# Kernel optimization log

Hardware: AMD Instinct MI355X
Metric: run time of the kernel (lower is better)

The kernel has to match this reference:

```python
import jax, jax.numpy as jnp
import numpy as np

DIL = 2  # dilation of the 3x3 neighborhood (hardcoded in the torch module)
# 8 non-center neighbor offsets of a dilated 3x3 kernel
_OFFSETS = [(-DIL, -DIL), (-DIL, 0), (-DIL, DIL),
            (0, -DIL),              (0, DIL),
            (DIL, -DIL), (DIL, 0),  (DIL, DIL)]


def setup_inputs() -> dict:
    key = jax.random.key(0)
    k1, k2 = jax.random.split(key)
    shape = (16, 1, 1024, 1024)
    y_true = jax.random.uniform(k1, shape, dtype=jnp.float32)
    y_pred = jax.random.uniform(k2, shape, dtype=jnp.float32)
    return {"y_true": y_true, "y_pred": y_pred}


def reference(y_true, y_pred):
    # --- BCE with torch's log clamp at -100 (reduction='none') ---
    log_p  = jnp.maximum(jnp.log(y_pred),   -100.0)
    log_1p = jnp.maximum(jnp.log1p(-y_pred), -100.0)
    a = -(y_true * log_p + (1.0 - y_true) * log_1p)

    # --- detached copy (y_pred.clone().detach()) ---
    sloss = jax.lax.stop_gradient(y_pred)

    # --- max |center - neighbor| over 8 dilated neighbors, zero-padded borders ---
    H, W = sloss.shape[2], sloss.shape[3]
    padded = jnp.pad(sloss, ((0, 0), (0, 0), (DIL, DIL), (DIL, DIL)))
    unfolded_weights = jnp.zeros_like(sloss)
    for dy, dx in _OFFSETS:
        nb = padded[:, :, DIL + dy:DIL + dy + H, DIL + dx:DIL + dx + W]
        unfolded_weights = jnp.maximum(unfolded_weights, jnp.abs(sloss - nb))

    # thred[thred < 0.5] = 0; loss1 uses thred BEFORE the >=0.5 -> 1 assignment
    thred = jnp.where(sloss >= 0.5, sloss, 0.0)
    loss = unfolded_weights * thred + a
    return loss.mean()
```

## Files before the change

kernel.cpp:

```cpp
#include <hip/hip_runtime.h>

#define HH 1024
#define WW 1024
#define NB 16
#define NROWS (NB * HH)
#define NELEM ((long long)NROWS * WW)

__global__ __launch_bounds__(256) void closs_main(const float* __restrict__ yt,
                                                  const float* __restrict__ yp,
                                                  float* __restrict__ partial) {
    __shared__ float up[1032];
    __shared__ float ce[1032];
    __shared__ float dn[1032];

    const int r   = blockIdx.x;
    const int y   = r & (HH - 1);
    const int tid = threadIdx.x;
    const int x4  = tid << 2;
    const long long rowbase = (long long)r * WW;

    if (tid < 4) {
        up[tid] = 0.f; ce[tid] = 0.f; dn[tid] = 0.f;
        up[1028 + tid] = 0.f; ce[1028 + tid] = 0.f; dn[1028 + tid] = 0.f;
    }

    float4 c4 = ((const float4*)(yp + rowbase))[tid];
    float4 u4 = make_float4(0.f, 0.f, 0.f, 0.f);
    float4 d4 = make_float4(0.f, 0.f, 0.f, 0.f);
    if (y >= 2)      u4 = ((const float4*)(yp + rowbase - 2 * WW))[tid];
    if (y < HH - 2)  d4 = ((const float4*)(yp + rowbase + 2 * WW))[tid];
    *(float4*)&ce[4 + x4] = c4;
    *(float4*)&up[4 + x4] = u4;
    *(float4*)&dn[4 + x4] = d4;
    __syncthreads();

    float sum = 0.f;
#pragma unroll
    for (int j = 0; j < 4; ++j) {
        const int x   = tid + (j << 8);
        const int idx = 4 + x;
        const float c = ce[idx];
        const float t = yt[rowbase + x];

        float w = fabsf(c - up[idx - 2]);
        w = fmaxf(w, fabsf(c - up[idx]));
        w = fmaxf(w, fabsf(c - up[idx + 2]));
        w = fmaxf(w, fabsf(c - ce[idx - 2]));
        w = fmaxf(w, fabsf(c - ce[idx + 2]));
        w = fmaxf(w, fabsf(c - dn[idx - 2]));
        w = fmaxf(w, fabsf(c - dn[idx]));
        w = fmaxf(w, fabsf(c - dn[idx + 2]));

        const float lp  = fmaxf(__logf(c), -100.f);
        const float l1p = fmaxf(__logf(1.f - c), -100.f);
        const float a   = -(t * lp + (1.f - t) * l1p);
        const float th  = (c >= 0.5f) ? c : 0.f;
        sum += w * th + a;
    }

    for (int o = 32; o > 0; o >>= 1) sum += __shfl_down(sum, o);
    __shared__ float wsum[4];
    if ((tid & 63) == 0) wsum[tid >> 6] = sum;
    __syncthreads();
    if (tid == 0) partial[r] = wsum[0] + wsum[1] + wsum[2] + wsum[3];
}

__global__ __launch_bounds__(256) void closs_reduce(const float* __restrict__ partial,
                                                    float* __restrict__ out) {
    float s = 0.f;
    for (int i = threadIdx.x; i < NROWS; i += 256) s += partial[i];
    for (int o = 32; o > 0; o >>= 1) s += __shfl_down(s, o);
    __shared__ float wsum[4];
    if ((threadIdx.x & 63) == 0) wsum[threadIdx.x >> 6] = s;
    __syncthreads();
    if (threadIdx.x == 0)
        out[0] = (wsum[0] + wsum[1] + wsum[2] + wsum[3]) * (1.0f / (float)NELEM);
}

extern "C" void kernel_launch(void* const* d_in, const int* in_sizes, int n_in,
                              void* d_out, int out_size, void* d_ws, size_t ws_size,
                              hipStream_t stream) {
    const float* y_true = (const float*)d_in[0];
    const float* y_pred = (const float*)d_in[1];
    float* out = (float*)d_out;
    float* partial = (float*)d_ws;

    closs_main<<<NROWS, 256, 0, stream>>>(y_true, y_pred, partial);
    closs_reduce<<<1, 256, 0, stream>>>(partial, out);
}
```

Baseline: 162.7 us.

## Replace LDS staging with direct register loads of halo neighbors; vectorize final reduce

The main kernel drops the shared-memory row staging and __syncthreads. Each thread now loads its 4 contiguous elements plus 2-element halos from global memory (float2/float4) for the center, up and down rows, computes the dilated max-diff in registers, and reads y_true as a float4. The intent is to remove LDS traffic and the barrier, at the cost of some redundant, less aligned halo loads that the cache should absorb. The reduce kernel moves to 1024 threads with float4 loads to shorten the serial loop.

```diff
diff --git a/kernel.cpp b/kernel.cpp
--- a/kernel.cpp
+++ b/kernel.cpp
@@ -9,53 +9,89 @@
 __global__ __launch_bounds__(256) void closs_main(const float* __restrict__ yt,
                                                   const float* __restrict__ yp,
                                                   float* __restrict__ partial) {
-    __shared__ float up[1032];
-    __shared__ float ce[1032];
-    __shared__ float dn[1032];
-
     const int r   = blockIdx.x;
     const int y   = r & (HH - 1);
     const int tid = threadIdx.x;
-    const int x4  = tid << 2;
+    const int x0  = tid << 2;
     const long long rowbase = (long long)r * WW;
 
-    if (tid < 4) {
-        up[tid] = 0.f; ce[tid] = 0.f; dn[tid] = 0.f;
-        up[1028 + tid] = 0.f; ce[1028 + tid] = 0.f; dn[1028 + tid] = 0.f;
+    const bool has_up = (y >= 2);
+    const bool has_dn = (y < HH - 2);
+    const bool ledge  = (tid == 0);
+    const bool redge  = (tid == 255);
+
+    const int offL = ledge ? x0 : (x0 - 2);
+    const int offR = redge ? x0 : (x0 + 4);
+
+    const float* pce = yp + rowbase;
+    const float* pup = pce - 2 * WW;
+    const float* pdn = pce + 2 * WW;
+
+    float ce[8];
+    {
+        float2 a = *(const float2*)(pce + offL);
+        float4 b = *(const float4*)(pce + x0);
+        float2 c = *(const float2*)(pce + offR);
+        if (ledge) { a.x = 0.f; a.y = 0.f; }
+        if (redge) { c.x = 0.f; c.y = 0.f; }
+        ce[0]=a.x; ce[1]=a.y; ce[2]=b.x; ce[3]=b.y; ce[4]=b.z; ce[5]=b.w; ce[6]=c.x; ce[7]=c.y;
+    }
+    const float4 t4 = *(const float4*)(yt + rowbase + x0);
+
+    float w0, w1, w2, w3;
+    {
+        w0 = fmaxf(fabsf(ce[2] - ce[0]), fabsf(ce[2] - ce[4]));
+        w1 = fmaxf(fabsf(ce[3] - ce[1]), fabsf(ce[3] - ce[5]));
+        w2 = fmaxf(fabsf(ce[4] - ce[2]), fabsf(ce[4] - ce[6]));
+        w3 = fmaxf(fabsf(ce[5] - ce[3]), fabsf(ce[5] - ce[7]));
+    }
+    if (has_up) {
+        float2 a = *(const float2*)(pup + offL);
+        float4 b = *(const float4*)(pup + x0);
+        float2 c = *(const float2*)(pup + offR);
+        if (ledge) { a.x = 0.f; a.y = 0.f; }
+        if (redge) { c.x = 0.f; c.y = 0.f; }
+        float u[8] = {a.x, a.y, b.x, b.y, b.z, b.w, c.x, c.y};
+        w0 = fmaxf(w0, fmaxf(fabsf(ce[2]-u[0]), fmaxf(fabsf(ce[2]-u[2]), fabsf(ce[2]-u[4]))));
+        w1 = fmaxf(w1, fmaxf(fabsf(ce[3]-u[1]), fmaxf(fabsf(ce[3]-u[3]), fabsf(ce[3]-u[5]))));
+        w2 = fmaxf(w2, fmaxf(fabsf(ce[4]-u[2]), fmaxf(fabsf(ce[4]-u[4]), fabsf(ce[4]-u[6]))));
+        w3 = fmaxf(w3, fmaxf(fabsf(ce[5]-u[3]), fmaxf(fabsf(ce[5]-u[5]), fabsf(ce[5]-u[7]))));
+    } else {
+        w0 = fmaxf(w0, fabsf(ce[2]));
+        w1 = fmaxf(w1, fabsf(ce[3]));
+        w2 = fmaxf(w2, fabsf(ce[4]));
+        w3 = fmaxf(w3, fabsf(ce[5]));
+    }
+    if (has_dn) {
+        float2 a = *(const float2*)(pdn + offL);
+        float4 b = *(const float4*)(pdn + x0);
+        float2 c = *(const float2*)(pdn + offR);
+        if (ledge) { a.x = 0.f; a.y = 0.f; }
+        if (redge) { c.x = 0.f; c.y = 0.f; }
+        float d[8] = {a.x, a.y, b.x, b.y, b.z, b.w, c.x, c.y};
+        w0 = fmaxf(w0, fmaxf(fabsf(ce[2]-d[0]), fmaxf(fabsf(ce[2]-d[2]), fabsf(ce[2]-d[4]))));
+        w1 = fmaxf(w1, fmaxf(fabsf(ce[3]-d[1]), fmaxf(fabsf(ce[3]-d[3]), fabsf(ce[3]-d[5]))));
+        w2 = fmaxf(w2, fmaxf(fabsf(ce[4]-d[2]), fmaxf(fabsf(ce[4]-d[4]), fabsf(ce[4]-d[6]))));
+        w3 = fmaxf(w3, fmaxf(fabsf(ce[5]-d[3]), fmaxf(fabsf(ce[5]-d[5]), fabsf(ce[5]-d[7]))));
+    } else {
+        w0 = fmaxf(w0, fabsf(ce[2]));
+        w1 = fmaxf(w1, fabsf(ce[3]));
+        w2 = fmaxf(w2, fabsf(ce[4]));
+        w3 = fmaxf(w3, fabsf(ce[5]));
     }
 
-    float4 c4 = ((const float4*)(yp + rowbase))[tid];
-    float4 u4 = make_float4(0.f, 0.f, 0.f, 0.f);
-    float4 d4 = make_float4(0.f, 0.f, 0.f, 0.f);
-    if (y >= 2)      u4 = ((const float4*)(yp + rowbase - 2 * WW))[tid];
-    if (y < HH - 2)  d4 = ((const float4*)(yp + rowbase + 2 * WW))[tid];
-    *(float4*)&ce[4 + x4] = c4;
-    *(float4*)&up[4 + x4] = u4;
-    *(float4*)&dn[4 + x4] = d4;
-    __syncthreads();
-
     float sum = 0.f;
+    const float cc[4] = {ce[2], ce[3], ce[4], ce[5]};
+    const float tt[4] = {t4.x, t4.y, t4.z, t4.w};
+    const float ww[4] = {w0, w1, w2, w3};
 #pragma unroll
     for (int j = 0; j < 4; ++j) {
-        const int x   = tid + (j << 8);
-        const int idx = 4 + x;
-        const float c = ce[idx];
-        const float t = yt[rowbase + x];
-
-        float w = fabsf(c - up[idx - 2]);
-        w = fmaxf(w, fabsf(c - up[idx]));
-        w = fmaxf(w, fabsf(c - up[idx + 2]));
-        w = fmaxf(w, fabsf(c - ce[idx - 2]));
-        w = fmaxf(w, fabsf(c - ce[idx + 2]));
-        w = fmaxf(w, fabsf(c - dn[idx - 2]));
-        w = fmaxf(w, fabsf(c - dn[idx]));
-        w = fmaxf(w, fabsf(c - dn[idx + 2]));
-
+        const float c = cc[j];
         const float lp  = fmaxf(__logf(c), -100.f);
         const float l1p = fmaxf(__logf(1.f - c), -100.f);
-        const float a   = -(t * lp + (1.f - t) * l1p);
+        const float a   = -(tt[j] * lp + (1.f - tt[j]) * l1p);
         const float th  = (c >= 0.5f) ? c : 0.f;
-        sum += w * th + a;
+        sum += ww[j] * th + a;
     }
 
     for (int o = 32; o > 0; o >>= 1) sum += __shfl_down(sum, o);
@@ -65,16 +101,25 @@
     if (tid == 0) partial[r] = wsum[0] + wsum[1] + wsum[2] + wsum[3];
 }
 
-__global__ __launch_bounds__(256) void closs_reduce(const float* __restrict__ partial,
-                                                    float* __restrict__ out) {
+__global__ __launch_bounds__(1024) void closs_reduce(const float* __restrict__ partial,
+                                                     float* __restrict__ out) {
+    const float4* p4 = (const float4*)partial;
     float s = 0.f;
-    for (int i = threadIdx.x; i < NROWS; i += 256) s += partial[i];
+#pragma unroll
+    for (int i = 0; i < 4; ++i) {
+        float4 v = p4[threadIdx.x + (i << 10)];
+        s += (v.x + v.y) + (v.z + v.w);
+    }
     for (int o = 32; o > 0; o >>= 1) s += __shfl_down(s, o);
-    __shared__ float wsum[4];
+    __shared__ float wsum[16];
     if ((threadIdx.x & 63) == 0) wsum[threadIdx.x >> 6] = s;
     __syncthreads();
-    if (threadIdx.x == 0)
-        out[0] = (wsum[0] + wsum[1] + wsum[2] + wsum[3]) * (1.0f / (float)NELEM);
+    if (threadIdx.x == 0) {
+        float t = 0.f;
+#pragma unroll
+        for (int i = 0; i < 16; ++i) t += wsum[i];
+        out[0] = t * (1.0f / (float)NELEM);
+    }
 }
 
 extern "C" void kernel_launch(void* const* d_in, const int* in_sizes, int n_in,
@@ -86,5 +131,5 @@
     float* partial = (float*)d_ws;
 
     closs_main<<<NROWS, 256, 0, stream>>>(y_true, y_pred, partial);
-    closs_reduce<<<1, 256, 0, stream>>>(partial, out);
+    closs_reduce<<<1, 1024, 0, stream>>>(partial, out);
 }
```

New measurement: 148.0 us. 9.1% less time.

## Process multiple same-parity rows per block with register sliding window and atomic reduction

Applied to the files above, without the earlier changes.

Each block now handles eight rows of the same parity (stride 2) and keeps a three-row register window, so each y_pred row is loaded once per block instead of three times. Horizontal neighbours come from extra float2 loads, which replaces the shared-memory staging and the barrier. The eight absolute differences are replaced by one neighbourhood max/min pair, and the separate reduce kernel is replaced by a memset plus per-block float atomicAdd. The cost is fewer blocks, more registers per thread and a summation order that is no longer deterministic.

```diff
diff --git a/kernel.cpp b/kernel.cpp
--- a/kernel.cpp
+++ b/kernel.cpp
@@ -3,78 +3,92 @@
 #define HH 1024
 #define WW 1024
 #define NB 16
-#define NROWS (NB * HH)
-#define NELEM ((long long)NROWS * WW)
+#define KROWS 8
+#define NELEM ((long long)NB * HH * WW)
+
+__device__ __forceinline__ void load_row(const float* __restrict__ rowp, int x0,
+                                         bool ledge, bool redge,
+                                         int offL, int offR, float w[8]) {
+    float2 a = *(const float2*)(rowp + offL);
+    float4 b = *(const float4*)(rowp + x0);
+    float2 c = *(const float2*)(rowp + offR);
+    if (ledge) { a.x = 0.f; a.y = 0.f; }
+    if (redge) { c.x = 0.f; c.y = 0.f; }
+    w[0]=a.x; w[1]=a.y; w[2]=b.x; w[3]=b.y; w[4]=b.z; w[5]=b.w; w[6]=c.x; w[7]=c.y;
+}
+
+__device__ __forceinline__ void zero_row(float w[8]) {
+#pragma unroll
+    for (int i = 0; i < 8; ++i) w[i] = 0.f;
+}
 
 __global__ __launch_bounds__(256) void closs_main(const float* __restrict__ yt,
                                                   const float* __restrict__ yp,
-                                                  float* __restrict__ partial) {
-    __shared__ float up[1032];
-    __shared__ float ce[1032];
-    __shared__ float dn[1032];
+                                                  float* __restrict__ out) {
+    const int bid = blockIdx.x;
+    const int img = bid >> 7;
+    const int rem = bid & 127;
+    const int par = rem >> 6;
+    const int seg = rem & 63;
+    const int y0  = seg * (2 * KROWS) + par;
 
-    const int r   = blockIdx.x;
-    const int y   = r & (HH - 1);
     const int tid = threadIdx.x;
-    const int x4  = tid << 2;
-    const long long rowbase = (long long)r * WW;
+    const int x0  = tid << 2;
+    const bool ledge = (tid == 0);
+    const bool redge = (tid == 255);
+    const int offL = ledge ? x0 : (x0 - 2);
+    const int offR = redge ? x0 : (x0 + 4);
 
-    if (tid < 4) {
-        up[tid] = 0.f; ce[tid] = 0.f; dn[tid] = 0.f;
-        up[1028 + tid] = 0.f; ce[1028 + tid] = 0.f; dn[1028 + tid] = 0.f;
-    }
+    const float* __restrict__ ybase = yp + (long long)img * (HH * WW);
+    const float* __restrict__ tbase = yt + (long long)img * (HH * WW);
 
-    float4 c4 = ((const float4*)(yp + rowbase))[tid];
-    float4 u4 = make_float4(0.f, 0.f, 0.f, 0.f);
-    float4 d4 = make_float4(0.f, 0.f, 0.f, 0.f);
-    if (y >= 2)      u4 = ((const float4*)(yp + rowbase - 2 * WW))[tid];
-    if (y < HH - 2)  d4 = ((const float4*)(yp + rowbase + 2 * WW))[tid];
-    *(float4*)&ce[4 + x4] = c4;
-    *(float4*)&up[4 + x4] = u4;
-    *(float4*)&dn[4 + x4] = d4;
-    __syncthreads();
+    float win[3][8];
+    if (y0 >= 2) load_row(ybase + (y0 - 2) * WW, x0, ledge, redge, offL, offR, win[0]);
+    else         zero_row(win[0]);
+    load_row(ybase + y0 * WW, x0, ledge, redge, offL, offR, win[1]);
 
     float sum = 0.f;
 #pragma unroll
-    for (int j = 0; j < 4; ++j) {
-        const int x   = tid + (j << 8);
-        const int idx = 4 + x;
-        const float c = ce[idx];
-        const float t = yt[rowbase + x];
+    for (int k = 0; k < KROWS; ++k) {
+        const int y = y0 + 2 * k;
+        float* A = win[k % 3];
+        float* B = win[(k + 1) % 3];
+        float* C = win[(k + 2) % 3];
+        if (y + 2 < HH) load_row(ybase + (y + 2) * WW, x0, ledge, redge, offL, offR, C);
+        else            zero_row(C);
 
-        float w = fabsf(c - up[idx - 2]);
-        w = fmaxf(w, fabsf(c - up[idx]));
-        w = fmaxf(w, fabsf(c - up[idx + 2]));
-        w = fmaxf(w, fabsf(c - ce[idx - 2]));
-        w = fmaxf(w, fabsf(c - ce[idx + 2]));
-        w = fmaxf(w, fabsf(c - dn[idx - 2]));
-        w = fmaxf(w, fabsf(c - dn[idx]));
-        w = fmaxf(w, fabsf(c - dn[idx + 2]));
+        const float4 t4 = *(const float4*)(tbase + y * WW + x0);
+        const float tt[4] = {t4.x, t4.y, t4.z, t4.w};
 
-        const float lp  = fmaxf(__logf(c), -100.f);
-        const float l1p = fmaxf(__logf(1.f - c), -100.f);
-        const float a   = -(t * lp + (1.f - t) * l1p);
-        const float th  = (c >= 0.5f) ? c : 0.f;
-        sum += w * th + a;
+#pragma unroll
+        for (int j = 0; j < 4; ++j) {
+            const float c = B[j + 2];
+            float mx = fmaxf(fmaxf(A[j], A[j + 2]), A[j + 4]);
+            mx = fmaxf(fmaxf(mx, B[j]), B[j + 4]);
+            mx = fmaxf(fmaxf(mx, C[j]), C[j + 2]);
+            mx = fmaxf(mx, C[j + 4]);
+            float mn = fminf(fminf(A[j], A[j + 2]), A[j + 4]);
+            mn = fminf(fminf(mn, B[j]), B[j + 4]);
+            mn = fminf(fminf(mn, C[j]), C[j + 2]);
+            mn = fminf(mn, C[j + 4]);
+            const float w = fmaxf(mx - c, c - mn);
+
+            const float lp  = fmaxf(__logf(c), -100.f);
+            const float l1p = fmaxf(__logf(1.f - c), -100.f);
+            const float a   = -(tt[j] * lp + (1.f - tt[j]) * l1p);
+            const float th  = (c >= 0.5f) ? c : 0.f;
+            sum += w * th + a;
+        }
     }
 
     for (int o = 32; o > 0; o >>= 1) sum += __shfl_down(sum, o);
     __shared__ float wsum[4];
     if ((tid & 63) == 0) wsum[tid >> 6] = sum;
     __syncthreads();
-    if (tid == 0) partial[r] = wsum[0] + wsum[1] + wsum[2] + wsum[3];
-}
-
-__global__ __launch_bounds__(256) void closs_reduce(const float* __restrict__ partial,
-                                                    float* __restrict__ out) {
-    float s = 0.f;
-    for (int i = threadIdx.x; i < NROWS; i += 256) s += partial[i];
-    for (int o = 32; o > 0; o >>= 1) s += __shfl_down(s, o);
-    __shared__ float wsum[4];
-    if ((threadIdx.x & 63) == 0) wsum[threadIdx.x >> 6] = s;
-    __syncthreads();
-    if (threadIdx.x == 0)
-        out[0] = (wsum[0] + wsum[1] + wsum[2] + wsum[3]) * (1.0f / (float)NELEM);
+    if (tid == 0) {
+        const float total = wsum[0] + wsum[1] + wsum[2] + wsum[3];
+        atomicAdd(out, total * (1.0f / (float)NELEM));
+    }
 }
 
 extern "C" void kernel_launch(void* const* d_in, const int* in_sizes, int n_in,
@@ -83,8 +97,7 @@
     const float* y_true = (const float*)d_in[0];
     const float* y_pred = (const float*)d_in[1];
     float* out = (float*)d_out;
-    float* partial = (float*)d_ws;
 
-    closs_main<<<NROWS, 256, 0, stream>>>(y_true, y_pred, partial);
-    closs_reduce<<<1, 256, 0, stream>>>(partial, out);
+    hipMemsetAsync(out, 0, sizeof(float), stream);
+    closs_main<<<NB * 2 * (HH / 2 / KROWS), 256, 0, stream>>>(y_true, y_pred, out);
 }
```

Result: faster. 147.9 us (-9.1%).
